# Optimization experiments

Hardware: AMD Instinct MI355X
Metric: run time of the kernel (lower is better)

## Reference

```python
import jax, jax.numpy as jnp
import numpy as np

N = 50000
E = 600000
LLM_DIM = 640
HIDDEN = 128
STRUCT_DIM = 16
N_STRUCT_TYPES = 5
N_LAYERS = 2
LN_EPS = 1e-5


def setup_inputs() -> dict:
    key = jax.random.key(0)
    ks = jax.random.split(key, 10)
    llm_feat = jax.random.normal(ks[0], (N, LLM_DIM), dtype=jnp.float32)
    struct_type_ids = jax.random.randint(ks[1], (N,), 0, N_STRUCT_TYPES, dtype=jnp.int64)
    edge_index = jax.random.randint(ks[2], (2, E), 0, N, dtype=jnp.int64)
    proj_out = HIDDEN - STRUCT_DIM  # 112
    proj_W = jax.random.normal(ks[3], (LLM_DIM, proj_out), dtype=jnp.float32) / np.sqrt(LLM_DIM)
    proj_b = jnp.zeros((proj_out,), dtype=jnp.float32)
    struct_emb = jax.random.normal(ks[4], (N_STRUCT_TYPES, STRUCT_DIM), dtype=jnp.float32)
    gcn_W = jax.random.normal(ks[5], (N_LAYERS, HIDDEN, HIDDEN), dtype=jnp.float32) / np.sqrt(HIDDEN)
    gcn_b = jnp.zeros((N_LAYERS, HIDDEN), dtype=jnp.float32)
    ln_g = jnp.ones((HIDDEN,), dtype=jnp.float32)
    ln_b = jnp.zeros((HIDDEN,), dtype=jnp.float32)
    return dict(llm_feat=llm_feat, struct_type_ids=struct_type_ids, edge_index=edge_index,
                proj_W=proj_W, proj_b=proj_b, struct_emb=struct_emb,
                gcn_W=gcn_W, gcn_b=gcn_b, ln_g=ln_g, ln_b=ln_b)


def _gcn_conv(x, src, dst, deg_inv_sqrt, W, b):
    """PyG GCNConv: x' = D^{-1/2}(A+I)D^{-1/2} (x W) + b, D over A+I."""
    xw = x @ W  # [N, H]
    norm = deg_inv_sqrt[src] * deg_inv_sqrt[dst]  # [E]
    msg = xw[src] * norm[:, None]  # [E, H]
    agg = jax.ops.segment_sum(msg, dst, num_segments=N)  # [N, H]
    # self-loop contribution: norm_ii = deg_i^{-1}
    agg = agg + xw * (deg_inv_sqrt * deg_inv_sqrt)[:, None]
    return agg + b


def reference(llm_feat, struct_type_ids, edge_index, proj_W, proj_b,
              struct_emb, gcn_W, gcn_b, ln_g, ln_b):
    x_llm = llm_feat @ proj_W + proj_b  # [N, hidden-struct_dim]
    x_struct = struct_emb[struct_type_ids]  # [N, struct_dim]
    x = jnp.concatenate([x_llm, x_struct], axis=-1)  # [N, hidden]

    src, dst = edge_index[0], edge_index[1]
    # degree with self-loops (A + I)
    deg = 1.0 + jax.ops.segment_sum(jnp.ones((E,), dtype=x.dtype), dst, num_segments=N)
    deg_inv_sqrt = jax.lax.rsqrt(deg)

    for l in range(N_LAYERS):
        x_new = jax.nn.relu(_gcn_conv(x, src, dst, deg_inv_sqrt, gcn_W[l], gcn_b[l]))
        # dropout is identity in eval mode
        x = x + x_new

    mean = jnp.mean(x, axis=-1, keepdims=True)
    var = jnp.mean(jnp.square(x - mean), axis=-1, keepdims=True)
    return (x - mean) * jax.lax.rsqrt(var + LN_EPS) * ln_g + ln_b
```

## Files before the change

### kernel.cpp

```cpp
#include <hip/hip_runtime.h>

#define N_NODES 50000
#define E_EDGES 600000
#define LLM_DIM 640
#define HIDDEN 128
#define POUT 112
#define NB_SCAN 98

typedef __attribute__((ext_vector_type(8))) short bf16x8;
typedef __attribute__((ext_vector_type(4))) float f32x4;

__device__ inline unsigned short f2bf(float f) {
    unsigned u = __float_as_uint(f);
    u += 0x7fff + ((u >> 16) & 1);
    return (unsigned short)(u >> 16);
}
__device__ inline float bflo(unsigned v) { return __uint_as_float(v << 16); }
__device__ inline float bfhi(unsigned v) { return __uint_as_float(v & 0xffff0000u); }

__global__ void deg_count(const int* __restrict__ eidx, int* __restrict__ cnt) {
    int e = blockIdx.x * 256 + threadIdx.x;
    if (e < E_EDGES) atomicAdd(&cnt[eidx[E_EDGES + e]], 1);
}

__global__ void make_dis(const int* __restrict__ cnt, float* __restrict__ dis) {
    int i = blockIdx.x * 256 + threadIdx.x;
    if (i < N_NODES) dis[i] = rsqrtf(1.0f + (float)cnt[i]);
}

__global__ __launch_bounds__(256) void scan_blocksum(const int* __restrict__ cnt, int* __restrict__ bsum) {
    __shared__ int s[256];
    int b = blockIdx.x, t = threadIdx.x;
    int i0 = b * 512 + t, i1 = i0 + 256;
    int v = (i0 < N_NODES ? cnt[i0] : 0) + (i1 < N_NODES ? cnt[i1] : 0);
    s[t] = v;
    __syncthreads();
    for (int st = 128; st; st >>= 1) {
        if (t < st) s[t] += s[t + st];
        __syncthreads();
    }
    if (t == 0) bsum[b] = s[0];
}

__global__ void scan_bsum(const int* __restrict__ bsum, int* __restrict__ bpre) {
    __shared__ int s[128];
    int t = threadIdx.x;
    if (t < NB_SCAN) s[t] = bsum[t];
    __syncthreads();
    if (t == 0) {
        int a = 0;
        for (int i = 0; i < NB_SCAN; i++) { int v = s[i]; s[i] = a; a += v; }
    }
    __syncthreads();
    if (t < NB_SCAN) bpre[t] = s[t];
}

__global__ __launch_bounds__(256) void scan_offs(const int* __restrict__ cnt, const int* __restrict__ bpre,
                                                 int* __restrict__ offs) {
    __shared__ int sA[512], sB[512];
    int b = blockIdx.x, t = threadIdx.x;
    int i0 = b * 512 + t, i1 = i0 + 256;
    int v0 = (i0 < N_NODES ? cnt[i0] : 0);
    int v1 = (i1 < N_NODES ? cnt[i1] : 0);
    sA[t] = v0; sA[t + 256] = v1;
    int* src = sA; int* dst = sB;
    for (int st = 1; st < 512; st <<= 1) {
        __syncthreads();
        dst[t]       = src[t]       + (t       >= st ? src[t - st]       : 0);
        dst[t + 256] = src[t + 256] + (t + 256 >= st ? src[t + 256 - st] : 0);
        int* tmp = src; src = dst; dst = tmp;
    }
    __syncthreads();
    int base = bpre[b];
    if (i0 < N_NODES) offs[i0] = base + src[t] - v0;
    if (i1 < N_NODES) offs[i1] = base + src[t + 256] - v1;
    if (b == 0 && t == 0) offs[N_NODES] = E_EDGES;
}

__global__ void fill_srcs(const int* __restrict__ eidx, const int* __restrict__ offs,
                          int* __restrict__ pos, int* __restrict__ srcs) {
    int e = blockIdx.x * 256 + threadIdx.x;
    if (e >= E_EDGES) return;
    int s = eidx[e];
    int d = eidx[E_EDGES + e];
    int p = atomicAdd(&pos[d], 1);
    srcs[offs[d] + p] = s;
}

__global__ void wt_convert(const float* __restrict__ W, unsigned short* __restrict__ Wt) {
    int idx = blockIdx.x * 256 + threadIdx.x;
    if (idx >= POUT * LLM_DIM) return;
    int n = idx / LLM_DIM;
    int k = idx - n * LLM_DIM;
    Wt[(size_t)n * LLM_DIM + k] = f2bf(W[(size_t)k * POUT + n]);
}

__global__ void w2_convert(const float* __restrict__ W, unsigned short* __restrict__ Wt2) {
    int idx = blockIdx.x * 256 + threadIdx.x;
    if (idx >= 2 * HIDDEN * HIDDEN) return;
    int l = idx >> 14;
    int rem = idx & 16383;
    int n = rem >> 7;
    int k = rem & 127;
    Wt2[idx] = f2bf(W[l * 16384 + k * 128 + n]);
}

__global__ __launch_bounds__(256) void proj_mfma(const float* __restrict__ A,
                                                 const unsigned short* __restrict__ Wt,
                                                 const float* __restrict__ bias,
                                                 const float* __restrict__ emb,
                                                 const int* __restrict__ sid,
                                                 const float* __restrict__ dis,
                                                 float* __restrict__ X,
                                                 unsigned short* __restrict__ Xs) {
    __shared__ short As[64][72];
    __shared__ short Bs[112][72];
    const int tid = threadIdx.x;
    const int wave = tid >> 6, lane = tid & 63;
    const int row0 = blockIdx.x * 64;
    const int l15 = lane & 15, l4 = lane >> 4;

    f32x4 acc[7];
#pragma unroll
    for (int j = 0; j < 7; j++) acc[j] = (f32x4){0.f, 0.f, 0.f, 0.f};

    for (int k0 = 0; k0 < LLM_DIM; k0 += 64) {
#pragma unroll
        for (int i = 0; i < 4; i++) {
            int f = i * 256 + tid;
            int r = f >> 4;
            int q = f & 15;
            int grow = row0 + r;
            float4 v = make_float4(0.f, 0.f, 0.f, 0.f);
            if (grow < N_NODES)
                v = *reinterpret_cast<const float4*>(A + (size_t)grow * LLM_DIM + k0 + q * 4);
            uint2 u;
            u.x = (unsigned)f2bf(v.x) | ((unsigned)f2bf(v.y) << 16);
            u.y = (unsigned)f2bf(v.z) | ((unsigned)f2bf(v.w) << 16);
            *reinterpret_cast<uint2*>(&As[r][q * 4]) = u;
        }
#pragma unroll
        for (int i = 0; i < 7; i++) {
            int f = i * 256 + tid;
            int n = f >> 4;
            int q = f & 15;
            uint2 v = *reinterpret_cast<const uint2*>(Wt + (size_t)n * LLM_DIM + k0 + q * 4);
            *reinterpret_cast<uint2*>(&Bs[n][q * 4]) = v;
        }
        __syncthreads();
#pragma unroll
        for (int ks = 0; ks < 2; ks++) {
            int kk = ks * 32 + l4 * 8;
            bf16x8 a = *reinterpret_cast<bf16x8*>(&As[wave * 16 + l15][kk]);
#pragma unroll
            for (int ct = 0; ct < 7; ct++) {
                bf16x8 b = *reinterpret_cast<bf16x8*>(&Bs[ct * 16 + l15][kk]);
                acc[ct] = __builtin_amdgcn_mfma_f32_16x16x32_bf16(a, b, acc[ct], 0, 0, 0);
            }
        }
        __syncthreads();
    }
#pragma unroll
    for (int r = 0; r < 4; r++) {
        int row = row0 + wave * 16 + l4 * 4 + r;
        if (row >= N_NODES) continue;
        float d = dis[row];
#pragma unroll
        for (int ct = 0; ct < 7; ct++) {
            int col = ct * 16 + l15;
            float v = acc[ct][r] + bias[col];
            X[(size_t)row * HIDDEN + col] = v;
            Xs[(size_t)row * HIDDEN + col] = f2bf(d * v);
        }
        float e = emb[sid[row] * 16 + l15];
        X[(size_t)row * HIDDEN + POUT + l15] = e;
        Xs[(size_t)row * HIDDEN + POUT + l15] = f2bf(d * e);
    }
}

__global__ __launch_bounds__(256) void gather(const unsigned short* __restrict__ Xs,
                                              const int* __restrict__ offs,
                                              const int* __restrict__ srcs,
                                              const float* __restrict__ dis,
                                              unsigned short* __restrict__ Gb) {
    int node = blockIdx.x * 4 + (threadIdx.x >> 6);
    int lane = threadIdx.x & 63;
    if (node >= N_NODES) return;
    int beg = __builtin_amdgcn_readfirstlane(offs[node]);
    int end = __builtin_amdgcn_readfirstlane(offs[node + 1]);
    const unsigned* X32 = reinterpret_cast<const unsigned*>(Xs);
    float ax = 0.f, ay = 0.f;
    int e = beg;
    while (e < end) {
        int n = end - e;
        if (n > 64) n = 64;
        int idx = (lane < n) ? srcs[e + lane] : 0;
        int j = 0;
        for (; j + 4 <= n; j += 4) {
            int s0 = __shfl(idx, j);
            int s1 = __shfl(idx, j + 1);
            int s2 = __shfl(idx, j + 2);
            int s3 = __shfl(idx, j + 3);
            unsigned v0 = X32[(size_t)s0 * 64 + lane];
            unsigned v1 = X32[(size_t)s1 * 64 + lane];
            unsigned v2 = X32[(size_t)s2 * 64 + lane];
            unsigned v3 = X32[(size_t)s3 * 64 + lane];
            ax += (bflo(v0) + bflo(v1)) + (bflo(v2) + bflo(v3));
            ay += (bfhi(v0) + bfhi(v1)) + (bfhi(v2) + bfhi(v3));
        }
        for (; j < n; j++) {
            int s = __shfl(idx, j);
            unsigned v = X32[(size_t)s * 64 + lane];
            ax += bflo(v);
            ay += bfhi(v);
        }
        e += 64;
    }
    float d = dis[node];
    unsigned sv = X32[(size_t)node * 64 + lane];
    ax = d * (ax + bflo(sv));
    ay = d * (ay + bfhi(sv));
    reinterpret_cast<unsigned*>(Gb)[(size_t)node * 64 + lane] =
        (unsigned)f2bf(ax) | ((unsigned)f2bf(ay) << 16);
}

template <int MODE>
__global__ __launch_bounds__(256) void gemm_fin(const unsigned short* __restrict__ Gb,
                                                const unsigned short* __restrict__ Wt2,
                                                const float* __restrict__ bias,
                                                const float* __restrict__ dis,
                                                const float* __restrict__ lng,
                                                const float* __restrict__ lnb,
                                                float* __restrict__ X,
                                                unsigned short* __restrict__ Xs2) {
    __shared__ short As[64][136];
    __shared__ short Bs[128][136];
    const int tid = threadIdx.x;
    const int wave = tid >> 6, lane = tid & 63;
    const int row0 = blockIdx.x * 64;
    const int l15 = lane & 15, l4 = lane >> 4;

#pragma unroll
    for (int i = 0; i < 4; i++) {
        int f = i * 256 + tid;
        int r = f >> 4;
        int q = f & 15;
        int grow = row0 + r;
        uint4 v = make_uint4(0, 0, 0, 0);
        if (grow < N_NODES)
            v = reinterpret_cast<const uint4*>(Gb + (size_t)grow * HIDDEN)[q];
        *reinterpret_cast<uint4*>(&As[r][q * 8]) = v;
    }
#pragma unroll
    for (int i = 0; i < 8; i++) {
        int f = i * 256 + tid;
        int r = f >> 4;
        int q = f & 15;
        uint4 v = reinterpret_cast<const uint4*>(Wt2 + (size_t)r * HIDDEN)[q];
        *reinterpret_cast<uint4*>(&Bs[r][q * 8]) = v;
    }
    __syncthreads();

    f32x4 acc[8];
#pragma unroll
    for (int j = 0; j < 8; j++) acc[j] = (f32x4){0.f, 0.f, 0.f, 0.f};
#pragma unroll
    for (int ks = 0; ks < 4; ks++) {
        int kk = ks * 32 + l4 * 8;
        bf16x8 a = *reinterpret_cast<bf16x8*>(&As[wave * 16 + l15][kk]);
#pragma unroll
        for (int ct = 0; ct < 8; ct++) {
            bf16x8 b = *reinterpret_cast<bf16x8*>(&Bs[ct * 16 + l15][kk]);
            acc[ct] = __builtin_amdgcn_mfma_f32_16x16x32_bf16(a, b, acc[ct], 0, 0, 0);
        }
    }

    float bcol[8];
#pragma unroll
    for (int ct = 0; ct < 8; ct++) bcol[ct] = bias[ct * 16 + l15];

    float vv[8][4];
#pragma unroll
    for (int r = 0; r < 4; r++) {
        int row = row0 + wave * 16 + l4 * 4 + r;
        bool ok = row < N_NODES;
#pragma unroll
        for (int ct = 0; ct < 8; ct++) {
            float xo = ok ? X[(size_t)row * HIDDEN + ct * 16 + l15] : 0.f;
            vv[ct][r] = xo + fmaxf(acc[ct][r] + bcol[ct], 0.f);
        }
    }

    if (MODE == 0) {
#pragma unroll
        for (int r = 0; r < 4; r++) {
            int row = row0 + wave * 16 + l4 * 4 + r;
            if (row >= N_NODES) continue;
            float d = dis[row];
#pragma unroll
            for (int ct = 0; ct < 8; ct++) {
                int col = ct * 16 + l15;
                X[(size_t)row * HIDDEN + col] = vv[ct][r];
                Xs2[(size_t)row * HIDDEN + col] = f2bf(d * vv[ct][r]);
            }
        }
    } else {
        float s[4], q2[4];
#pragma unroll
        for (int r = 0; r < 4; r++) {
            s[r] = 0.f; q2[r] = 0.f;
#pragma unroll
            for (int ct = 0; ct < 8; ct++) {
                s[r] += vv[ct][r];
                q2[r] += vv[ct][r] * vv[ct][r];
            }
        }
#pragma unroll
        for (int off = 1; off < 16; off <<= 1) {
#pragma unroll
            for (int r = 0; r < 4; r++) {
                s[r] += __shfl_xor(s[r], off);
                q2[r] += __shfl_xor(q2[r], off);
            }
        }
        float gcol[8], bcol2[8];
#pragma unroll
        for (int ct = 0; ct < 8; ct++) {
            gcol[ct] = lng[ct * 16 + l15];
            bcol2[ct] = lnb[ct * 16 + l15];
        }
#pragma unroll
        for (int r = 0; r < 4; r++) {
            int row = row0 + wave * 16 + l4 * 4 + r;
            if (row >= N_NODES) continue;
            float mean = s[r] * (1.f / 128.f);
            float var = q2[r] * (1.f / 128.f) - mean * mean;
            float inv = rsqrtf(var + 1e-5f);
#pragma unroll
            for (int ct = 0; ct < 8; ct++) {
                int col = ct * 16 + l15;
                X[(size_t)row * HIDDEN + col] = (vv[ct][r] - mean) * inv * gcol[ct] + bcol2[ct];
            }
        }
    }
}

extern "C" void kernel_launch(void* const* d_in, const int* in_sizes, int n_in,
                              void* d_out, int out_size, void* d_ws, size_t ws_size,
                              hipStream_t stream) {
    const float* llm   = (const float*)d_in[0];
    const int*   sid   = (const int*)d_in[1];
    const int*   eidx  = (const int*)d_in[2];
    const float* projW = (const float*)d_in[3];
    const float* projb = (const float*)d_in[4];
    const float* emb   = (const float*)d_in[5];
    const float* gcnW  = (const float*)d_in[6];
    const float* gcnb  = (const float*)d_in[7];
    const float* lng   = (const float*)d_in[8];
    const float* lnb   = (const float*)d_in[9];

    float* X = (float*)d_out;
    unsigned short* Xs = (unsigned short*)d_ws;
    unsigned short* Gb = Xs + (size_t)N_NODES * HIDDEN;
    unsigned short* Wt = Gb;
    unsigned short* Wt2 = Gb + (size_t)N_NODES * HIDDEN;
    float* dis = (float*)(Wt2 + 2 * HIDDEN * HIDDEN);
    int* cnt  = (int*)(dis + N_NODES);
    int* offs = cnt + N_NODES;
    int* bsum = offs + N_NODES + 1;
    int* bpre = bsum + 128;
    int* srcs = bpre + 128;

    hipMemsetAsync(cnt, 0, N_NODES * sizeof(int), stream);
    deg_count<<<(E_EDGES + 255) / 256, 256, 0, stream>>>(eidx, cnt);
    make_dis<<<(N_NODES + 255) / 256, 256, 0, stream>>>(cnt, dis);
    scan_blocksum<<<NB_SCAN, 256, 0, stream>>>(cnt, bsum);
    scan_bsum<<<1, 128, 0, stream>>>(bsum, bpre);
    scan_offs<<<NB_SCAN, 256, 0, stream>>>(cnt, bpre, offs);
    hipMemsetAsync(cnt, 0, N_NODES * sizeof(int), stream);
    fill_srcs<<<(E_EDGES + 255) / 256, 256, 0, stream>>>(eidx, offs, cnt, srcs);

    wt_convert<<<(POUT * LLM_DIM + 255) / 256, 256, 0, stream>>>(projW, Wt);
    w2_convert<<<(2 * HIDDEN * HIDDEN + 255) / 256, 256, 0, stream>>>(gcnW, Wt2);

    proj_mfma<<<(N_NODES + 63) / 64, 256, 0, stream>>>(llm, Wt, projb, emb, sid, dis, X, Xs);

    gather<<<(N_NODES + 3) / 4, 256, 0, stream>>>(Xs, offs, srcs, dis, Gb);
    gemm_fin<0><<<(N_NODES + 63) / 64, 256, 0, stream>>>(Gb, Wt2, gcnb, dis, lng, lnb, X, Xs);
    gather<<<(N_NODES + 3) / 4, 256, 0, stream>>>(Xs, offs, srcs, dis, Gb);
    gemm_fin<1><<<(N_NODES + 63) / 64, 256, 0, stream>>>(Gb, Wt2 + HIDDEN * HIDDEN, gcnb + HIDDEN, dis, lng, lnb, X, Xs);
}
```

Before: 389.5 us.

## Load projection GEMM operands straight from global into registers without LDS

Removes the shared-memory staging tiles and block barriers from the projection MFMA kernel. Each lane now reads its A fragment (fp32, converted to bf16 in registers) and its B fragments directly from global memory, with the next A chunk prefetched through a two-stage register double buffer. The aim is to drop LDS round-trips and __syncthreads stalls in this memory-bound GEMM. In exchange, A reads are 32-byte strided per lane and less coalesced, and every wave re-reads the whole weight matrix from cache.

```diff
diff --git a/kernel.cpp b/kernel.cpp
--- a/kernel.cpp
+++ b/kernel.cpp
@@ -113,53 +113,48 @@
                                                  const float* __restrict__ dis,
                                                  float* __restrict__ X,
                                                  unsigned short* __restrict__ Xs) {
-    __shared__ short As[64][72];
-    __shared__ short Bs[112][72];
     const int tid = threadIdx.x;
     const int wave = tid >> 6, lane = tid & 63;
+    const int l15 = lane & 15, l4 = lane >> 4;
     const int row0 = blockIdx.x * 64;
-    const int l15 = lane & 15, l4 = lane >> 4;
+
+    int arow = row0 + wave * 16 + l15;
+    if (arow >= N_NODES) arow = N_NODES - 1;
+    const float* Ap = A + (size_t)arow * LLM_DIM + l4 * 8;
+    const unsigned short* Bp = Wt + (size_t)l15 * LLM_DIM + l4 * 8;
 
     f32x4 acc[7];
 #pragma unroll
     for (int j = 0; j < 7; j++) acc[j] = (f32x4){0.f, 0.f, 0.f, 0.f};
 
-    for (int k0 = 0; k0 < LLM_DIM; k0 += 64) {
-#pragma unroll
-        for (int i = 0; i < 4; i++) {
-            int f = i * 256 + tid;
-            int r = f >> 4;
-            int q = f & 15;
-            int grow = row0 + r;
-            float4 v = make_float4(0.f, 0.f, 0.f, 0.f);
-            if (grow < N_NODES)
-                v = *reinterpret_cast<const float4*>(A + (size_t)grow * LLM_DIM + k0 + q * 4);
-            uint2 u;
-            u.x = (unsigned)f2bf(v.x) | ((unsigned)f2bf(v.y) << 16);
-            u.y = (unsigned)f2bf(v.z) | ((unsigned)f2bf(v.w) << 16);
-            *reinterpret_cast<uint2*>(&As[r][q * 4]) = u;
-        }
-#pragma unroll
-        for (int i = 0; i < 7; i++) {
-            int f = i * 256 + tid;
-            int n = f >> 4;
-            int q = f & 15;
-            uint2 v = *reinterpret_cast<const uint2*>(Wt + (size_t)n * LLM_DIM + k0 + q * 4);
-            *reinterpret_cast<uint2*>(&Bs[n][q * 4]) = v;
-        }
-        __syncthreads();
-#pragma unroll
-        for (int ks = 0; ks < 2; ks++) {
-            int kk = ks * 32 + l4 * 8;
-            bf16x8 a = *reinterpret_cast<bf16x8*>(&As[wave * 16 + l15][kk]);
-#pragma unroll
-            for (int ct = 0; ct < 7; ct++) {
-                bf16x8 b = *reinterpret_cast<bf16x8*>(&Bs[ct * 16 + l15][kk]);
-                acc[ct] = __builtin_amdgcn_mfma_f32_16x16x32_bf16(a, b, acc[ct], 0, 0, 0);
-            }
-        }
-        __syncthreads();
-    }
+    float4 a[2][2];
+    a[0][0] = *reinterpret_cast<const float4*>(Ap);
+    a[0][1] = *reinterpret_cast<const float4*>(Ap + 4);
+
+#pragma unroll
+    for (int t = 0; t < 20; t++) {
+        const int cur = t & 1, nxt = cur ^ 1;
+        if (t < 19) {
+            const int k1 = (t + 1) * 32;
+            a[nxt][0] = *reinterpret_cast<const float4*>(Ap + k1);
+            a[nxt][1] = *reinterpret_cast<const float4*>(Ap + k1 + 4);
+        }
+        bf16x8 b[7];
+        const int k0 = t * 32;
+#pragma unroll
+        for (int ct = 0; ct < 7; ct++)
+            b[ct] = *reinterpret_cast<const bf16x8*>(Bp + (size_t)ct * 16 * LLM_DIM + k0);
+        bf16x8 av;
+        unsigned* ap = reinterpret_cast<unsigned*>(&av);
+        ap[0] = (unsigned)f2bf(a[cur][0].x) | ((unsigned)f2bf(a[cur][0].y) << 16);
+        ap[1] = (unsigned)f2bf(a[cur][0].z) | ((unsigned)f2bf(a[cur][0].w) << 16);
+        ap[2] = (unsigned)f2bf(a[cur][1].x) | ((unsigned)f2bf(a[cur][1].y) << 16);
+        ap[3] = (unsigned)f2bf(a[cur][1].z) | ((unsigned)f2bf(a[cur][1].w) << 16);
+#pragma unroll
+        for (int ct = 0; ct < 7; ct++)
+            acc[ct] = __builtin_amdgcn_mfma_f32_16x16x32_bf16(av, b[ct], acc[ct], 0, 0, 0);
+    }
+
 #pragma unroll
     for (int r = 0; r < 4; r++) {
         int row = row0 + wave * 16 + l4 * 4 + r;
```

Result: slower. 434.5 us (+11.5%).
